# Performance work log

Hardware: AMD Instinct MI355X
Metric: run time of the kernel (lower is better)

The kernel has to match this reference:

```python
import jax, jax.numpy as jnp
import numpy as np
from jax import lax

B, L, D = 2, 1024, 1024
INTER = 2816  # _find_multiple(round(4.0*1024*2/3), 256)
K, PAD = 3, 1
S = 32  # sqrt(L)
K2 = K * K


def setup_inputs() -> dict:
    key = jax.random.key(0)
    ks = jax.random.split(key, 7)
    x = jax.random.normal(ks[0], (B, L, D), dtype=jnp.float32)
    w_gate_up = jax.random.normal(ks[1], (2 * INTER, D), dtype=jnp.float32) / np.sqrt(D)
    w_metric = jax.random.normal(ks[2], (7, INTER, 3, 3), dtype=jnp.float32) / np.sqrt(INTER * 9)
    b_metric = jax.random.normal(ks[3], (7,), dtype=jnp.float32) * 0.01
    conv_w = jax.random.normal(ks[4], (INTER, 1, K, K), dtype=jnp.float32) / K
    conv_b = jnp.zeros((INTER,), dtype=jnp.float32)
    w_down = jax.random.normal(ks[5], (D, INTER), dtype=jnp.float32) / np.sqrt(INTER)
    return {"x": x, "w_gate_up": w_gate_up, "w_metric": w_metric,
            "b_metric": b_metric, "conv_w": conv_w, "conv_b": conv_b,
            "w_down": w_down}


def _metric_offsets(x2d, w_metric, b_metric):
    # Finsler-Randers style metric: 2x2 linear map M, drift vector, tanh scale.
    p = lax.conv_general_dilated(x2d, w_metric, (1, 1), 'SAME',
                                 dimension_numbers=('NCHW', 'OIHW', 'NCHW'))
    p = p + b_metric[None, :, None, None]  # [B,7,S,S]
    m00, m01, m10, m11 = p[:, 0], p[:, 1], p[:, 2], p[:, 3]
    dr_y, dr_x = p[:, 4], p[:, 5]
    scale = jnp.tanh(p[:, 6])
    ky = (jnp.arange(K) - PAD).astype(x2d.dtype)
    py = jnp.repeat(ky, K)   # (K2,) kernel-tap dy
    px = jnp.tile(ky, K)     # (K2,) kernel-tap dx
    pyb = py[None, :, None, None]
    pxb = px[None, :, None, None]
    off_y = scale[:, None] * (m00[:, None] * pyb + m01[:, None] * pxb) + dr_y[:, None]
    off_x = scale[:, None] * (m10[:, None] * pyb + m11[:, None] * pxb) + dr_x[:, None]
    return off_y, off_x, py, px  # offsets: [B,K2,S,S]


def _deform_depthwise(x2d, off_y, off_x, py, px, conv_w, conv_b):
    # Sampling positions per output pixel & kernel tap: [B,K2,S,S]
    iy = jnp.arange(S, dtype=x2d.dtype)
    pos_y = iy[None, None, :, None] + py[None, :, None, None] + off_y
    pos_x = iy[None, None, None, :] + px[None, :, None, None] + off_x
    y0 = jnp.floor(pos_y)
    x0 = jnp.floor(pos_x)
    ty = pos_y - y0
    tx = pos_x - x0
    y0i = y0.astype(jnp.int32)
    x0i = x0.astype(jnp.int32)
    flat = x2d.reshape(B, INTER, S * S)

    def corner(yy, xx):
        valid = ((yy >= 0) & (yy < S) & (xx >= 0) & (xx < S)).astype(x2d.dtype)
        idx = (jnp.clip(yy, 0, S - 1) * S + jnp.clip(xx, 0, S - 1)).reshape(B, 1, -1)
        v = jnp.take_along_axis(flat, idx, axis=2).reshape(B, INTER, K2, S, S)
        return v * valid[:, None]

    w00 = ((1 - ty) * (1 - tx))[:, None]
    w01 = ((1 - ty) * tx)[:, None]
    w10 = (ty * (1 - tx))[:, None]
    w11 = (ty * tx)[:, None]
    acc = w00 * corner(y0i, x0i)
    acc = acc + w01 * corner(y0i, x0i + 1)
    acc = acc + w10 * corner(y0i + 1, x0i)
    acc = acc + w11 * corner(y0i + 1, x0i + 1)
    out = jnp.einsum('bckij,ck->bcij', acc, conv_w.reshape(INTER, K2))
    return out + conv_b[None, :, None, None]


def reference(x, w_gate_up, w_metric, b_metric, conv_w, conv_b, w_down):
    gu = jnp.einsum('bld,fd->blf', x, w_gate_up)          # [B,L,2*inter]
    gate, up = jnp.split(gu, 2, axis=-1)
    x_ffn = jax.nn.silu(gate) * up                         # [B,L,inter]
    x2d = x_ffn.transpose(0, 2, 1).reshape(B, INTER, S, S)
    off_y, off_x, py, px = _metric_offsets(x2d, w_metric, b_metric)
    out2d = _deform_depthwise(x2d, off_y, off_x, py, px, conv_w, conv_b)
    grid_out = out2d.reshape(B, INTER, L).transpose(0, 2, 1)
    return jnp.einsum('blf,df->bld', grid_out, w_down)
```

## Files before the change

### kernel.cpp

```cpp
#include <hip/hip_runtime.h>
#include <hip/hip_bf16.h>
#include <cstdint>
#include <cstddef>
#include <type_traits>

#define INTER 2816

typedef __bf16 bf16x8 __attribute__((ext_vector_type(8)));
typedef float f32x4 __attribute__((ext_vector_type(4)));
typedef unsigned short u16x8 __attribute__((ext_vector_type(8)));
using bf16 = __hip_bfloat16;
using u16 = unsigned short;

__device__ __forceinline__ u16 f2bu(float f) {
  bf16 h = __float2bfloat16(f);
  return *reinterpret_cast<u16*>(&h);
}
__device__ __forceinline__ float bu2f(u16 u) {
  bf16 h = *reinterpret_cast<bf16*>(&u);
  return __bfloat162float(h);
}

__device__ __forceinline__ void async16(const u16* g, u16* l) {
  __builtin_amdgcn_global_load_lds(
      (const __attribute__((address_space(1))) unsigned int*)g,
      (__attribute__((address_space(3))) unsigned int*)l, 16, 0, 0);
}

__device__ __forceinline__ void stage8(u16* dst, const float* src) {
  const float4 a = *(const float4*)(src);
  const float4 b = *(const float4*)(src + 4);
  u16 tmp[8] = {f2bu(a.x), f2bu(a.y), f2bu(a.z), f2bu(a.w),
                f2bu(b.x), f2bu(b.y), f2bu(b.z), f2bu(b.w)};
  *(uint4*)dst = *(uint4*)tmp;
}

__global__ __launch_bounds__(256)
void prep_all(const float* __restrict__ x, const float* __restrict__ wgu,
              const float* __restrict__ wd, const float* __restrict__ w_metric,
              const float* __restrict__ conv_w, u16* __restrict__ xbf,
              u16* __restrict__ wgubf, u16* __restrict__ wdbf,
              u16* __restrict__ wm2, u16* __restrict__ cwb) {
  constexpr size_t S0 = (size_t)2048 * 1024;
  constexpr size_t S1 = (size_t)5632 * 1024;
  constexpr size_t S2 = (size_t)1024 * 2816;
  constexpr size_t NCONV_THREADS = (S0 + S1 + S2) / 8;
  const size_t t = (size_t)blockIdx.x * 256 + threadIdx.x;
  if (t < NCONV_THREADS) {
    const size_t e0 = t * 8;
    const float* src;
    u16* dst;
    size_t off;
    if (e0 < S0) {
      src = x; dst = xbf; off = e0;
    } else if (e0 < S0 + S1) {
      src = wgu; dst = wgubf; off = e0 - S0;
    } else {
      src = wd; dst = wdbf; off = e0 - S0 - S1;
    }
    stage8(dst + off, src + off);
  } else {
    const unsigned p = (unsigned)(t - NCONV_THREADS);
    const unsigned y = p / 2816u;
    const unsigned c = p - y * 2816u;
    if (y < 64) {
      float v = 0.f;
      if (y < 63) {
        const unsigned o = y / 9, tap = y - o * 9;
        v = w_metric[((size_t)o * INTER + c) * 9 + tap];
      }
      wm2[(size_t)y * INTER + c] = f2bu(v);
    } else {
      const unsigned k = y - 64;
      cwb[(size_t)k * INTER + c] = f2bu(conv_w[(size_t)c * 9 + k]);
    }
  }
}

template <int BN, bool NSWAP, typename OT>
__global__ __launch_bounds__(256, 3)
void gemm_nt(const u16* __restrict__ A, int lda, const u16* __restrict__ Bt,
             int ldb, OT* __restrict__ C, int M, int ldc, int K) {
  constexpr int NJ = BN / 32;
  constexpr int BHALF = BN * 32;
  __shared__ u16 As[2 * 128 * 32];
  __shared__ u16 Bs[2 * BHALF];
  const size_t koff = (size_t)blockIdx.z * K;
  A += koff;
  Bt += koff;
  C += (size_t)blockIdx.z * M * ldc;
  const int m0 = (NSWAP ? blockIdx.y : blockIdx.x) * 128;
  const int n0 = (NSWAP ? blockIdx.x : blockIdx.y) * BN;
  const int tid = threadIdx.x;
  const int lane = tid & 63;
  const int wv = tid >> 6;
  const int wm = wv & 1, wn = wv >> 1;
  const int lr = lane & 15;
  const int lq = lane >> 4;

  f32x4 acc[4][NJ];
#pragma unroll
  for (int i = 0; i < 4; ++i)
#pragma unroll
    for (int j = 0; j < NJ; ++j) acc[i][j] = (f32x4){0.f, 0.f, 0.f, 0.f};

  const int srow = tid >> 2;
  const int scol = (tid & 3) * 8;
  const u16* gA0 = A + (size_t)(m0 + srow) * lda + scol;
  const u16* gA1 = A + (size_t)(m0 + 64 + srow) * lda + scol;
  const u16* gB0 = Bt + (size_t)(n0 + srow) * ldb + scol;
  const u16* gB1 = Bt + (size_t)(n0 + 64 + srow) * ldb + scol;

  for (int kb = 0; kb < K; kb += 64) {
#pragma unroll
    for (int h = 0; h < 2; ++h) {
      const int kh = kb + h * 32;
      async16(gA0 + kh, As + h * 4096 + tid * 8);
      async16(gA1 + kh, As + h * 4096 + 2048 + tid * 8);
      async16(gB0 + kh, Bs + h * BHALF + tid * 8);
      if constexpr (BN == 128) async16(gB1 + kh, Bs + h * BHALF + 2048 + tid * 8);
    }
    __syncthreads();
#pragma unroll
    for (int h = 0; h < 2; ++h) {
      bf16x8 af[4], bfr[NJ];
#pragma unroll
      for (int i = 0; i < 4; ++i)
        af[i] = *(const bf16x8*)(&As[h * 4096 + (wm * 64 + i * 16 + lr) * 32 + lq * 8]);
#pragma unroll
      for (int j = 0; j < NJ; ++j)
        bfr[j] = *(const bf16x8*)(&Bs[h * BHALF + (wn * (BN / 2) + j * 16 + lr) * 32 + lq * 8]);
#pragma unroll
      for (int i = 0; i < 4; ++i)
#pragma unroll
        for (int j = 0; j < NJ; ++j)
          acc[i][j] = __builtin_amdgcn_mfma_f32_16x16x32_bf16(af[i], bfr[j],
                                                              acc[i][j], 0, 0, 0);
    }
    __syncthreads();
  }

#pragma unroll
  for (int i = 0; i < 4; ++i)
#pragma unroll
    for (int j = 0; j < NJ; ++j) {
      const int col = n0 + wn * (BN / 2) + j * 16 + lr;
#pragma unroll
      for (int r = 0; r < 4; ++r) {
        const int row = m0 + wm * 64 + i * 16 + lq * 4 + r;
        const float v = acc[i][j][r];
        if constexpr (std::is_same_v<OT, float>) {
          C[(size_t)row * ldc + col] = v;
        } else {
          C[(size_t)row * ldc + col] = f2bu(v);
        }
      }
    }
}

__global__ __launch_bounds__(256, 3)
void gateup_gemm(const u16* __restrict__ x, const u16* __restrict__ wgu,
                 u16* __restrict__ xffn) {
  constexpr int K = 1024;
  __shared__ u16 As[2 * 128 * 32];
  __shared__ u16 Bgs[2 * 64 * 32];
  __shared__ u16 Bus[2 * 64 * 32];
  const int n0 = blockIdx.x * 64;
  const int m0 = blockIdx.y * 128;
  const int tid = threadIdx.x;
  const int lane = tid & 63;
  const int wv = tid >> 6;
  const int wm = wv & 1, wn = wv >> 1;
  const int lr = lane & 15;
  const int lq = lane >> 4;

  f32x4 accg[4][2], accu[4][2];
#pragma unroll
  for (int i = 0; i < 4; ++i)
#pragma unroll
    for (int j = 0; j < 2; ++j) {
      accg[i][j] = (f32x4){0.f, 0.f, 0.f, 0.f};
      accu[i][j] = (f32x4){0.f, 0.f, 0.f, 0.f};
    }

  const int srow = tid >> 2;
  const int scol = (tid & 3) * 8;
  const u16* gA0 = x + (size_t)(m0 + srow) * K + scol;
  const u16* gA1 = x + (size_t)(m0 + 64 + srow) * K + scol;
  const u16* gBg = wgu + (size_t)(n0 + srow) * K + scol;
  const u16* gBu = wgu + (size_t)(INTER + n0 + srow) * K + scol;

  for (int kb = 0; kb < K; kb += 64) {
#pragma unroll
    for (int h = 0; h < 2; ++h) {
      const int kh = kb + h * 32;
      async16(gA0 + kh, As + h * 4096 + tid * 8);
      async16(gA1 + kh, As + h * 4096 + 2048 + tid * 8);
      async16(gBg + kh, Bgs + h * 2048 + tid * 8);
      async16(gBu + kh, Bus + h * 2048 + tid * 8);
    }
    __syncthreads();
#pragma unroll
    for (int h = 0; h < 2; ++h) {
      bf16x8 af[4], bg[2], bu[2];
#pragma unroll
      for (int i = 0; i < 4; ++i)
        af[i] = *(const bf16x8*)(&As[h * 4096 + (wm * 64 + i * 16 + lr) * 32 + lq * 8]);
#pragma unroll
      for (int j = 0; j < 2; ++j) {
        bg[j] = *(const bf16x8*)(&Bgs[h * 2048 + (wn * 32 + j * 16 + lr) * 32 + lq * 8]);
        bu[j] = *(const bf16x8*)(&Bus[h * 2048 + (wn * 32 + j * 16 + lr) * 32 + lq * 8]);
      }
#pragma unroll
      for (int i = 0; i < 4; ++i)
#pragma unroll
        for (int j = 0; j < 2; ++j) {
          accg[i][j] = __builtin_amdgcn_mfma_f32_16x16x32_bf16(af[i], bg[j],
                                                               accg[i][j], 0, 0, 0);
          accu[i][j] = __builtin_amdgcn_mfma_f32_16x16x32_bf16(af[i], bu[j],
                                                               accu[i][j], 0, 0, 0);
        }
    }
    __syncthreads();
  }

#pragma unroll
  for (int i = 0; i < 4; ++i)
#pragma unroll
    for (int j = 0; j < 2; ++j) {
      const int col = n0 + wn * 32 + j * 16 + lr;
#pragma unroll
      for (int r = 0; r < 4; ++r) {
        const int row = m0 + wm * 64 + i * 16 + lq * 4 + r;
        const float g = accg[i][j][r];
        const float u = accu[i][j][r];
        const float s = g / (1.f + __expf(-g));
        xffn[(size_t)row * INTER + col] = f2bu(s * u);
      }
    }
}

__global__ __launch_bounds__(64)
void offsets_fused(const float* __restrict__ q,
                   const float* __restrict__ b_metric,
                   float4* __restrict__ wrec, int4* __restrict__ orec) {
  __shared__ float lds[130 * 65];
  const int chunk = blockIdx.x;
  const int b = chunk >> 4;
  const int c0 = (chunk & 15) * 64;
  const int t = threadIdx.x;

  for (int v = t; v < 130 * 16; v += 64) {
    const int row = v >> 4;
    const int c4 = (v & 15) * 4;
    int pg = c0 - 33 + row;
    pg = min(max(pg, 0), 1023);
    const float* src = q + ((size_t)b * 1024 + pg) * 64 + c4;
    float4 s = *(const float4*)(src);
#pragma unroll
    for (int ks = 1; ks < 11; ++ks) {
      const float4 vv = *(const float4*)(src + (size_t)ks * 2048 * 64);
      s.x += vv.x; s.y += vv.y; s.z += vv.z; s.w += vv.w;
    }
    float* d = &lds[row * 65 + c4];
    d[0] = s.x; d[1] = s.y; d[2] = s.z; d[3] = s.w;
  }
  __syncthreads();

  const int pix = c0 + t;
  const int i = pix >> 5, j = pix & 31;
  float p[7];
#pragma unroll
  for (int o = 0; o < 7; ++o) p[o] = b_metric[o];
#pragma unroll
  for (int tap = 0; tap < 9; ++tap) {
    const int dy = tap / 3 - 1, dx = tap % 3 - 1;
    const int ii = i + dy, jj = j + dx;
    if ((unsigned)ii < 32u && (unsigned)jj < 32u) {
      const float* r = &lds[(t + 33 + dy * 32 + dx) * 65 + tap];
#pragma unroll
      for (int o = 0; o < 7; ++o) p[o] += r[o * 9];
    }
  }
  const float m00 = p[0], m01 = p[1], m10 = p[2], m11 = p[3];
  const float dry = p[4], drx = p[5];
  const float sc = tanhf(p[6]);
#pragma unroll
  for (int k = 0; k < 9; ++k) {
    const float pyk = (float)(k / 3 - 1), pxk = (float)(k % 3 - 1);
    const float offy = sc * (m00 * pyk + m01 * pxk) + dry;
    const float offx = sc * (m10 * pyk + m11 * pxk) + drx;
    const float posy = (float)i + pyk + offy;
    const float posx = (float)j + pxk + offx;
    const float y0f = floorf(posy), x0f = floorf(posx);
    const int y0 = (int)y0f, x0 = (int)x0f;
    const float ty = posy - y0f, tx = posx - x0f;
    const int y1 = y0 + 1, x1 = x0 + 1;
    const float vy0 = ((unsigned)y0 < 32u) ? 1.f : 0.f;
    const float vy1 = ((unsigned)y1 < 32u) ? 1.f : 0.f;
    const float vx0 = ((unsigned)x0 < 32u) ? 1.f : 0.f;
    const float vx1 = ((unsigned)x1 < 32u) ? 1.f : 0.f;
    float4 w;
    w.x = (1.f - ty) * (1.f - tx) * vy0 * vx0;
    w.y = (1.f - ty) * tx * vy0 * vx1;
    w.z = ty * (1.f - tx) * vy1 * vx0;
    w.w = ty * tx * vy1 * vx1;
    const int cy0 = min(max(y0, 0), 31), cy1 = min(max(y1, 0), 31);
    const int cx0 = min(max(x0, 0), 31), cx1 = min(max(x1, 0), 31);
    int4 o;
    o.x = (cy0 * 32 + cx0) * (INTER * 2);
    o.y = (cy0 * 32 + cx1) * (INTER * 2);
    o.z = (cy1 * 32 + cx0) * (INTER * 2);
    o.w = (cy1 * 32 + cx1) * (INTER * 2);
    const size_t r = (((size_t)b * 9 + k) << 10) + pix;
    wrec[r] = w;
    orec[r] = o;
  }
}

__global__ __launch_bounds__(256)
void deform_kernel(const u16* __restrict__ xffn,
                   const float4* __restrict__ wrec,
                   const int4* __restrict__ orec,
                   const u16* __restrict__ cwb,
                   const float* __restrict__ conv_b,
                   u16* __restrict__ gridout) {
  const unsigned bid = (blockIdx.x & 7u) * 352u + (blockIdx.x >> 3);
  const unsigned t = bid * 256 + threadIdx.x;
  const unsigned pix = t / 352u;
  const unsigned cv = t - pix * 352u;
  const int c0 = cv * 8;
  const int b = pix >> 10, l = pix & 1023;

  float acc[8];
  {
    const float4 b0 = *(const float4*)(&conv_b[c0]);
    const float4 b1 = *(const float4*)(&conv_b[c0 + 4]);
    acc[0] = b0.x; acc[1] = b0.y; acc[2] = b0.z; acc[3] = b0.w;
    acc[4] = b1.x; acc[5] = b1.y; acc[6] = b1.z; acc[7] = b1.w;
  }
  const char* xb = (const char*)xffn +
                   ((size_t)b * 1024 * INTER + c0) * sizeof(u16);
#pragma unroll
  for (int k = 0; k < 9; ++k) {
    const size_t r = (((size_t)b * 9 + k) << 10) + l;
    const float4 w = wrec[r];
    const int4 o = orec[r];
    const u16x8 v00 = *(const u16x8*)(xb + o.x);
    const u16x8 v01 = *(const u16x8*)(xb + o.y);
    const u16x8 v10 = *(const u16x8*)(xb + o.z);
    const u16x8 v11 = *(const u16x8*)(xb + o.w);
    const u16x8 cw = *(const u16x8*)(&cwb[(size_t)k * INTER + c0]);
#pragma unroll
    for (int e = 0; e < 8; ++e) {
      const float bl = w.x * bu2f(v00[e]) + w.y * bu2f(v01[e]) +
                       w.z * bu2f(v10[e]) + w.w * bu2f(v11[e]);
      acc[e] += bl * bu2f(cw[e]);
    }
  }
  u16 outv[8];
#pragma unroll
  for (int e = 0; e < 8; ++e) outv[e] = f2bu(acc[e]);
  *(uint4*)(gridout + ((size_t)b * 1024 + l) * INTER + c0) = *(uint4*)outv;
}

extern "C" void kernel_launch(void* const* d_in, const int* in_sizes, int n_in,
                              void* d_out, int out_size, void* d_ws,
                              size_t ws_size, hipStream_t stream) {
  const float* x         = (const float*)d_in[0];
  const float* w_gate_up = (const float*)d_in[1];
  const float* w_metric  = (const float*)d_in[2];
  const float* b_metric  = (const float*)d_in[3];
  const float* conv_w    = (const float*)d_in[4];
  const float* conv_b    = (const float*)d_in[5];
  const float* w_down    = (const float*)d_in[6];
  float* out = (float*)d_out;

  char* w = (char*)d_ws;
  u16* gridout  = (u16*)(w);
  u16* xffn     = (u16*)(w + (12u << 20));
  u16* xbf      = (u16*)(w + (24u << 20));
  u16* wgubf    = (u16*)(w + (28u << 20) + (256u << 10));
  float* q_conv = (float*)(w + (28u << 20) + (256u << 10));
  u16* wm2      = (u16*)(w + (40u << 20));
  u16* cwb      = (u16*)(w + (41u << 20));
  float4* wrec  = (float4*)(w + (42u << 20));
  int4* orec    = (int4*)(w + (43u << 20));
  u16* wdbf     = (u16*)(w + (44u << 20));

  prep_all<<<6051, 256, 0, stream>>>(x, w_gate_up, w_down, w_metric, conv_w,
                                     xbf, wgubf, wdbf, wm2, cwb);
  gateup_gemm<<<dim3(44, 16), 256, 0, stream>>>(xbf, wgubf, xffn);
  gemm_nt<64, false, float><<<dim3(16, 1, 11), 256, 0, stream>>>(
      xffn, INTER, wm2, INTER, q_conv, 2048, 64, 256);
  offsets_fused<<<32, 64, 0, stream>>>(q_conv, b_metric, wrec, orec);
  deform_kernel<<<2816, 256, 0, stream>>>(xffn, wrec, orec, cwb, conv_b,
                                          gridout);
  gemm_nt<64, true, float><<<dim3(16, 16), 256, 0, stream>>>(
      gridout, INTER, wdbf, INTER, out, 2048, 1024, 2816);
}
```

Baseline: 211.7 us.

## Split-K the down projection with atomic-counter fused reduction

The final down-projection GEMM becomes a 4-way split-K with 128-wide N tiles. Each split writes fp32 partials to a workspace that overlays the xffn buffer, and the last block to finish a tile, found through an atomic counter, sums the partials into the output. The aim is more blocks and better CU fill than the 256-block launch. It costs extra fp32 partial traffic and a memset. Smaller tweaks widen offsets_fused to 256 threads for its load phase and lower gateup_gemm's occupancy hint to 2.

```diff
diff --git a/kernel.cpp b/kernel.cpp
--- a/kernel.cpp
+++ b/kernel.cpp
@@ -77,18 +77,20 @@
   }
 }
 
-template <int BN, bool NSWAP, typename OT>
+template <int BN, bool NSWAP, bool REDUCE, typename OT>
 __global__ __launch_bounds__(256, 3)
 void gemm_nt(const u16* __restrict__ A, int lda, const u16* __restrict__ Bt,
-             int ldb, OT* __restrict__ C, int M, int ldc, int K) {
+             int ldb, OT* __restrict__ C, int M, int ldc, int K,
+             float* __restrict__ out, unsigned* __restrict__ cnt, int NZ) {
   constexpr int NJ = BN / 32;
   constexpr int BHALF = BN * 32;
   __shared__ u16 As[2 * 128 * 32];
   __shared__ u16 Bs[2 * BHALF];
+  __shared__ unsigned s_done;
   const size_t koff = (size_t)blockIdx.z * K;
   A += koff;
   Bt += koff;
-  C += (size_t)blockIdx.z * M * ldc;
+  OT* Cz = C + (size_t)blockIdx.z * M * ldc;
   const int m0 = (NSWAP ? blockIdx.y : blockIdx.x) * 128;
   const int n0 = (NSWAP ? blockIdx.x : blockIdx.y) * BN;
   const int tid = threadIdx.x;
@@ -150,15 +152,36 @@
         const int row = m0 + wm * 64 + i * 16 + lq * 4 + r;
         const float v = acc[i][j][r];
         if constexpr (std::is_same_v<OT, float>) {
-          C[(size_t)row * ldc + col] = v;
+          Cz[(size_t)row * ldc + col] = v;
         } else {
-          C[(size_t)row * ldc + col] = f2bu(v);
+          Cz[(size_t)row * ldc + col] = f2bu(v);
         }
       }
     }
-}
-
-__global__ __launch_bounds__(256, 3)
+
+  if constexpr (REDUCE) {
+    __threadfence();
+    const int tile = blockIdx.y * gridDim.x + blockIdx.x;
+    if (tid == 0) s_done = atomicAdd(&cnt[tile], 1u);
+    __syncthreads();
+    if (s_done != (unsigned)(NZ - 1)) return;
+    __threadfence();
+    const int nf4 = 128 * BN / 4;
+    for (int v = tid; v < nf4; v += 256) {
+      const int row = m0 + v / (BN / 4);
+      const int c4 = n0 + (v % (BN / 4)) * 4;
+      const float* p0 = (const float*)C + (size_t)row * ldc + c4;
+      float4 s = *(const float4*)(p0);
+      for (int z = 1; z < NZ; ++z) {
+        const float4 vv = *(const float4*)(p0 + (size_t)z * M * ldc);
+        s.x += vv.x; s.y += vv.y; s.z += vv.z; s.w += vv.w;
+      }
+      *(float4*)(out + (size_t)row * ldc + c4) = s;
+    }
+  }
+}
+
+__global__ __launch_bounds__(256, 2)
 void gateup_gemm(const u16* __restrict__ x, const u16* __restrict__ wgu,
                  u16* __restrict__ xffn) {
   constexpr int K = 1024;
@@ -240,7 +263,7 @@
     }
 }
 
-__global__ __launch_bounds__(64)
+__global__ __launch_bounds__(256)
 void offsets_fused(const float* __restrict__ q,
                    const float* __restrict__ b_metric,
                    float4* __restrict__ wrec, int4* __restrict__ orec) {
@@ -250,7 +273,7 @@
   const int c0 = (chunk & 15) * 64;
   const int t = threadIdx.x;
 
-  for (int v = t; v < 130 * 16; v += 64) {
+  for (int v = t; v < 130 * 16; v += 256) {
     const int row = v >> 4;
     const int c4 = (v & 15) * 4;
     int pg = c0 - 33 + row;
@@ -266,6 +289,7 @@
     d[0] = s.x; d[1] = s.y; d[2] = s.z; d[3] = s.w;
   }
   __syncthreads();
+  if (t >= 64) return;
 
   const int pix = c0 + t;
   const int i = pix >> 5, j = pix & 31;
@@ -378,6 +402,7 @@
 
   char* w = (char*)d_ws;
   u16* gridout  = (u16*)(w);
+  float* q2     = (float*)(w + (12u << 20));
   u16* xffn     = (u16*)(w + (12u << 20));
   u16* xbf      = (u16*)(w + (24u << 20));
   u16* wgubf    = (u16*)(w + (28u << 20) + (256u << 10));
@@ -387,15 +412,17 @@
   float4* wrec  = (float4*)(w + (42u << 20));
   int4* orec    = (int4*)(w + (43u << 20));
   u16* wdbf     = (u16*)(w + (44u << 20));
-
+  unsigned* cnt = (unsigned*)(w + (49u << 20) + (900u << 10));
+
+  hipMemsetAsync(cnt, 0, 128 * sizeof(unsigned), stream);
   prep_all<<<6051, 256, 0, stream>>>(x, w_gate_up, w_down, w_metric, conv_w,
                                      xbf, wgubf, wdbf, wm2, cwb);
   gateup_gemm<<<dim3(44, 16), 256, 0, stream>>>(xbf, wgubf, xffn);
-  gemm_nt<64, false, float><<<dim3(16, 1, 11), 256, 0, stream>>>(
-      xffn, INTER, wm2, INTER, q_conv, 2048, 64, 256);
-  offsets_fused<<<32, 64, 0, stream>>>(q_conv, b_metric, wrec, orec);
+  gemm_nt<64, false, false, float><<<dim3(16, 1, 11), 256, 0, stream>>>(
+      xffn, INTER, wm2, INTER, q_conv, 2048, 64, 256, nullptr, nullptr, 11);
+  offsets_fused<<<32, 256, 0, stream>>>(q_conv, b_metric, wrec, orec);
   deform_kernel<<<2816, 256, 0, stream>>>(xffn, wrec, orec, cwb, conv_b,
                                           gridout);
-  gemm_nt<64, true, float><<<dim3(16, 16), 256, 0, stream>>>(
-      gridout, INTER, wdbf, INTER, out, 2048, 1024, 2816);
-}
+  gemm_nt<128, true, true, float><<<dim3(8, 16, 4), 256, 0, stream>>>(
+      gridout, INTER, wdbf, INTER, q2, 2048, 1024, 704, out, cnt, 4);
+}
```

After: 280.6 us. 1.33x slower.
